# Performance work log

Measured on AMD Instinct MI355X. Metric: run time of the kernel, lower is better.

Reference implementation:

```python
import jax, jax.numpy as jnp
import numpy as np

D_MODEL, D_STATE, D_CONV, EXPAND = 1024, 16, 4, 2
D_INNER = D_MODEL * EXPAND
BATCH, SEQ = 2, 2048


def setup_inputs() -> dict:
    key = jax.random.key(0)
    ks = jax.random.split(key, 10)
    s = lambda d: 1.0 / np.sqrt(d)
    return {
        "x": jax.random.normal(ks[0], (BATCH, SEQ, D_MODEL), jnp.float32),
        "norm_w": jnp.ones((D_MODEL,), jnp.float32),
        "norm_b": jnp.zeros((D_MODEL,), jnp.float32),
        "W_in": jax.random.normal(ks[1], (2 * D_INNER, D_MODEL), jnp.float32) * s(D_MODEL),
        "conv_w": jax.random.normal(ks[2], (D_INNER, D_CONV), jnp.float32) * s(D_CONV),
        "conv_b": jnp.zeros((D_INNER,), jnp.float32),
        "W_dt": jax.random.normal(ks[3], (D_INNER, D_INNER), jnp.float32) * s(D_INNER),
        "b_dt": jnp.zeros((D_INNER,), jnp.float32),
        "W_B": jax.random.normal(ks[4], (D_STATE, D_INNER), jnp.float32) * s(D_INNER),
        "W_C": jax.random.normal(ks[5], (D_STATE, D_INNER), jnp.float32) * s(D_INNER),
        "D": jnp.ones((D_INNER,), jnp.float32),
        "A_log": jnp.broadcast_to(jnp.log(jnp.arange(1, D_STATE + 1, dtype=jnp.float32)), (D_INNER, D_STATE)),
        "W_out": jax.random.normal(ks[6], (D_MODEL, D_INNER), jnp.float32) * s(D_INNER),
    }


def _layernorm(x, w, b, eps=1e-5):
    mu = jnp.mean(x, axis=-1, keepdims=True)
    var = jnp.var(x, axis=-1, keepdims=True)
    return (x - mu) * jax.lax.rsqrt(var + eps) * w + b


def _causal_depthwise_conv(x, w, b):
    # x: [B, L, C], w: [C, K], b: [C]; torch Conv1d(padding=K-1) then slice [:L] == left-pad causal conv
    K = w.shape[1]
    xp = jnp.pad(x, ((0, 0), (K - 1, 0), (0, 0)))
    L = x.shape[1]
    out = b
    for k in range(K):  # small fixed K=4
        out = out + xp[:, k:k + L, :] * w[:, k]
    return out


def reference(x, norm_w, norm_b, W_in, conv_w, conv_b, W_dt, b_dt, W_B, W_C, D, A_log, W_out):
    residual = x
    xn = _layernorm(x, norm_w, norm_b)
    xz = jnp.einsum("bld,ed->ble", xn, W_in)            # [B,L,2*d_inner]
    x_part, z = jnp.split(xz, 2, axis=-1)
    x_conv = jax.nn.silu(_causal_depthwise_conv(x_part, conv_w, conv_b))  # [B,L,di]
    dt = jax.nn.softplus(jnp.einsum("bld,ed->ble", x_conv, W_dt) + b_dt)  # [B,L,di]
    Bm = jnp.einsum("bld,nd->bln", x_conv, W_B)         # [B,L,ds]
    Cm = jnp.einsum("bld,nd->bln", x_conv, W_C)         # [B,L,ds]
    A = -jnp.exp(A_log)                                  # [di,ds]

    def step(h, inp):
        dt_t, B_t, C_t, xc_t = inp                       # [B,di],[B,ds],[B,ds],[B,di]
        h = h * jnp.exp(A[None] * dt_t[:, :, None]) + xc_t[:, :, None] * B_t[:, None, :] * dt_t[:, :, None]
        y_t = jnp.sum(h * C_t[:, None, :], axis=-1)      # [B,di]
        return h, y_t

    h0 = jnp.zeros((x.shape[0], A.shape[0], A.shape[1]), x_conv.dtype)
    # scan over time: move L to leading axis
    xs = (jnp.swapaxes(dt, 0, 1), jnp.swapaxes(Bm, 0, 1), jnp.swapaxes(Cm, 0, 1), jnp.swapaxes(x_conv, 0, 1))
    _, y = jax.lax.scan(step, h0, xs)                    # y: [L,B,di]
    y = jnp.swapaxes(y, 0, 1)
    y = y + x_conv * D
    y = y * jax.nn.silu(z)
    return residual + jnp.einsum("ble,de->bld", y, W_out)
```

## Files before the change

### kernel.cpp

```cpp
#include <hip/hip_runtime.h>
#include <cstdint>
#include <cstddef>

#define D_MODEL 1024
#define D_INNER 2048
#define D_STATE 16
#define SEQ     2048
#define NROWS   4096

typedef short short4v __attribute__((ext_vector_type(4)));
typedef short short8v __attribute__((ext_vector_type(8)));
typedef float float4v __attribute__((ext_vector_type(4)));

__device__ __forceinline__ float bf2f(short u) {
  union { unsigned int i; float f; } v;
  v.i = ((unsigned int)(unsigned short)u) << 16;
  return v.f;
}
__device__ __forceinline__ short f2bf(float f) {
  union { float f; unsigned int i; } v; v.f = f;
  unsigned int r = v.i + 0x7FFFu + ((v.i >> 16) & 1u);
  return (short)(r >> 16);
}
__device__ __forceinline__ float lde(const void* p, size_t i, int f32) {
  return f32 ? ((const float*)p)[i] : bf2f(((const short*)p)[i]);
}
__device__ __forceinline__ void async16(short* lds, const short* g) {
  __builtin_amdgcn_global_load_lds(
      (const __attribute__((address_space(1))) unsigned int*)g,
      (__attribute__((address_space(3))) unsigned int*)lds, 16, 0, 0);
}

__global__ __launch_bounds__(64) void probe_kernel(const unsigned int* __restrict__ xw,
                                                   int* __restrict__ flag) {
  int cnt = 0;
  for (int i = threadIdx.x; i < 1024; i += 64) {
    unsigned e = (xw[i] >> 7) & 0xFFu;
    cnt += (e >= 100u && e <= 150u) ? 1 : 0;
  }
  #pragma unroll
  for (int o = 32; o >= 1; o >>= 1) cnt += __shfl_xor(cnt, o);
  if (threadIdx.x == 0) *flag = (cnt < 614) ? 1 : 0;
}

#define WIN_N  4194304u
#define WDT_N  4194304u
#define WBC_N  32768u
#define WPAD_N 196608u
#define WCAT_N (WDT_N + 2u*WBC_N + WPAD_N)
#define WOUT_N 2097152u
__global__ __launch_bounds__(256) void cvt_kernel(
    const void* __restrict__ Win, const void* __restrict__ Wdt,
    const void* __restrict__ WBp, const void* __restrict__ WCp,
    const void* __restrict__ Wout, short* __restrict__ dst,
    const int* __restrict__ flag) {
  const int f32 = *flag;
  const size_t i = ((size_t)blockIdx.x * 256 + threadIdx.x) * 8;
  const void* src = nullptr; size_t off = 0; bool zero = false;
  if (i < WIN_N) { src = Win; off = i; }
  else {
    size_t j = i - WIN_N;
    if (j < WDT_N) { src = Wdt; off = j; }
    else {
      j -= WDT_N;
      if (j < WBC_N) { src = WBp; off = j; }
      else {
        j -= WBC_N;
        if (j < WBC_N) { src = WCp; off = j; }
        else {
          j -= WBC_N;
          if (j < WPAD_N) zero = true;
          else { src = Wout; off = j - WPAD_N; }
        }
      }
    }
  }
  short8v o;
  if (zero) {
    #pragma unroll
    for (int j = 0; j < 8; ++j) o[j] = 0;
  } else if (f32) {
    const float* s = (const float*)src + off;
    #pragma unroll
    for (int j = 0; j < 8; ++j) o[j] = f2bf(s[j]);
  } else {
    o = *(const short8v*)((const short*)src + off);
  }
  *(short8v*)&dst[i] = o;
}

__global__ __launch_bounds__(256) void ln_kernel(
    const void* __restrict__ x, const void* __restrict__ w,
    const void* __restrict__ bb, short* __restrict__ xn,
    const int* __restrict__ flag) {
  const int f32 = *flag;
  const int row = blockIdx.x;
  const int tid = threadIdx.x;
  float v0, v1, v2, v3;
  if (f32) {
    float4v xv = ((const float4v*)((const float*)x + (size_t)row * D_MODEL))[tid];
    v0 = xv[0]; v1 = xv[1]; v2 = xv[2]; v3 = xv[3];
  } else {
    short4v xv = *(const short4v*)&((const short*)x)[(size_t)row * D_MODEL + tid * 4];
    v0 = bf2f(xv[0]); v1 = bf2f(xv[1]); v2 = bf2f(xv[2]); v3 = bf2f(xv[3]);
  }
  float s = v0 + v1 + v2 + v3;
  float q = v0*v0 + v1*v1 + v2*v2 + v3*v3;
  #pragma unroll
  for (int off = 32; off >= 1; off >>= 1) {
    s += __shfl_xor(s, off);
    q += __shfl_xor(q, off);
  }
  __shared__ float red[8];
  const int wid = tid >> 6;
  if ((tid & 63) == 0) { red[wid] = s; red[4 + wid] = q; }
  __syncthreads();
  s = red[0] + red[1] + red[2] + red[3];
  q = red[4] + red[5] + red[6] + red[7];
  const float mu = s * (1.f / 1024.f);
  const float var = q * (1.f / 1024.f) - mu * mu;
  const float rstd = rsqrtf(var + 1e-5f);
  short4v ov;
  #pragma unroll
  for (int j = 0; j < 4; ++j) {
    const float vj = (j == 0) ? v0 : (j == 1) ? v1 : (j == 2) ? v2 : v3;
    const float o = (vj - mu) * rstd * lde(w, tid * 4 + j, f32) + lde(bb, tid * 4 + j, f32);
    ov[j] = f2bf(o);
  }
  *(short4v*)&xn[(size_t)row * D_MODEL + tid * 4] = ov;
}

template <int MODE, int BM>
__global__ __launch_bounds__(2 * BM) void gemm_bt(
    const short* __restrict__ A, int lda, const short* __restrict__ B,
    void* __restrict__ Cv, int N, int K, const void* __restrict__ aux,
    float* __restrict__ Bmo, float* __restrict__ Cmo,
    const int* __restrict__ flag) {
  constexpr int NBUF = (BM == 256) ? 2 : 4;
  __shared__ __align__(16) short As[NBUF][BM * 32];
  __shared__ __align__(16) short Bs[NBUF][128 * 32];
  const int f32 = *flag;
  const int tid = threadIdx.x;
  const int bm = blockIdx.y * BM;
  const int bn = blockIdx.x << 7;
  const int wid = tid >> 6;
  const int lane = tid & 63;
  const int wm = (wid >> 1) << 6;
  const int wn = (wid & 1) << 6;

  float4v acc[4][4];
  #pragma unroll
  for (int i = 0; i < 4; ++i)
    #pragma unroll
    for (int j = 0; j < 4; ++j) acc[i][j] = (float4v){0.f, 0.f, 0.f, 0.f};

  const int srow = tid >> 2;
  const int scol = (((tid & 3) ^ ((tid >> 3) & 3)) << 3);
  const short* ga = A + (size_t)(bm + srow) * lda + scol;
  const short* gb = B + (size_t)(bn + srow) * K + scol;
  const size_t astep = (size_t)(BM / 2) * lda;
  const size_t bstep = (size_t)64 * K;

  const int fr = lane & 15;
  const int fq = (((lane >> 4) ^ ((lane >> 1) & 3)) << 3);

#define STAGE(Ad, Bd, kk) do {                              \
    async16(&Ad[tid * 8], ga + (kk));                       \
    async16(&Ad[BM * 16 + tid * 8], ga + astep + (kk));     \
    if (BM == 256) {                                        \
      async16(&Bd[tid * 8], gb + (kk));                     \
    } else {                                                \
      async16(&Bd[tid * 8], gb + (kk));                     \
      async16(&Bd[2048 + tid * 8], gb + bstep + (kk));      \
    } } while (0)
#define VMW(NW) __builtin_amdgcn_s_waitcnt(0x3FF0 | (NW))
#define BAR __builtin_amdgcn_s_barrier()

  auto compute = [&](const short* Asrc, const short* Bsrc) {
    short8v af[4], bfv[4];
    #pragma unroll
    for (int i = 0; i < 4; ++i)
      af[i] = *(const short8v*)&Asrc[(wm + i * 16 + fr) * 32 + fq];
    #pragma unroll
    for (int j = 0; j < 4; ++j)
      bfv[j] = *(const short8v*)&Bsrc[(wn + j * 16 + fr) * 32 + fq];
    #pragma unroll
    for (int i = 0; i < 4; ++i)
      #pragma unroll
      for (int j = 0; j < 4; ++j)
        acc[i][j] = __builtin_amdgcn_mfma_f32_16x16x32_bf16(af[i], bfv[j], acc[i][j], 0, 0, 0);
  };

  const int nk = K >> 5;
  if constexpr (BM == 128) {
    STAGE(As[0], Bs[0], 0);
    STAGE(As[1], Bs[1], 32);
    STAGE(As[2], Bs[2], 64);
    int c = 0;
    for (; c + 4 < nk; c += 4) {
      STAGE(As[3], Bs[3], (c + 3) << 5); VMW(12); BAR; compute(As[0], Bs[0]); BAR;
      STAGE(As[0], Bs[0], (c + 4) << 5); VMW(12); BAR; compute(As[1], Bs[1]); BAR;
      STAGE(As[1], Bs[1], (c + 5) << 5); VMW(12); BAR; compute(As[2], Bs[2]); BAR;
      STAGE(As[2], Bs[2], (c + 6) << 5); VMW(12); BAR; compute(As[3], Bs[3]); BAR;
    }
    STAGE(As[3], Bs[3], (nk - 1) << 5); VMW(12); BAR; compute(As[0], Bs[0]); BAR;
    VMW(8); BAR; compute(As[1], Bs[1]); BAR;
    VMW(4); BAR; compute(As[2], Bs[2]); BAR;
    VMW(0); BAR; compute(As[3], Bs[3]);
  } else {
    constexpr int VM3 = 3;
    STAGE(As[0], Bs[0], 0);
    for (int k2 = 0; k2 < nk; k2 += 2) {
      STAGE(As[1], Bs[1], (k2 + 1) << 5);
      VMW(VM3);
      BAR;
      compute(As[0], Bs[0]);
      BAR;
      if (k2 + 2 < nk) {
        STAGE(As[0], Bs[0], (k2 + 2) << 5);
        VMW(VM3);
      } else {
        VMW(0);
      }
      BAR;
      compute(As[1], Bs[1]);
      BAR;
    }
  }
#undef STAGE
#undef VMW
#undef BAR

  const int er = (lane >> 4) << 2;
  const int ec = lane & 15;
  #pragma unroll
  for (int i = 0; i < 4; ++i) {
    #pragma unroll
    for (int j = 0; j < 4; ++j) {
      const int gcol = bn + wn + j * 16 + ec;
      #pragma unroll
      for (int r = 0; r < 4; ++r) {
        const int grow = bm + wm + i * 16 + er + r;
        float v = acc[i][j][r];
        if (MODE == 1) {
          if (gcol < 2048) {
            v += lde(aux, gcol, f32);
            v = (v > 15.f) ? v : log1pf(__expf(v));
            ((short*)Cv)[(size_t)grow * 2048 + gcol] = f2bf(v);
          } else if (gcol < 2064) {
            Bmo[(size_t)grow * 16 + (gcol - 2048)] = v;
          } else if (gcol < 2080) {
            Cmo[(size_t)grow * 16 + (gcol - 2064)] = v;
          }
        } else {
          const size_t idx = (size_t)grow * N + gcol;
          if (MODE == 2) {
            v += lde(aux, idx, f32);
            if (f32) ((float*)Cv)[idx] = v;
            else     ((short*)Cv)[idx] = f2bf(v);
          } else {
            ((short*)Cv)[idx] = f2bf(v);
          }
        }
      }
    }
  }
}

__global__ __launch_bounds__(256) void bc_kernel(
    const short* __restrict__ xcv, const short* __restrict__ wbc,
    float* __restrict__ Bmo, float* __restrict__ Cmo) {
  const int tid = threadIdx.x;
  const int w = tid >> 6;
  const int lane = tid & 63;
  const int fr = lane & 15;
  const int hi = lane >> 4;
  const int r0 = blockIdx.x << 4;
  const short* ap  = xcv + (size_t)(r0 + fr) * 2048 + hi * 8;
  const short* b0p = wbc + (size_t)fr * 2048 + hi * 8;
  const short* b1p = wbc + (size_t)(16 + fr) * 2048 + hi * 8;
  float4v acc0 = (float4v){0.f, 0.f, 0.f, 0.f};
  float4v acc1 = (float4v){0.f, 0.f, 0.f, 0.f};
  #pragma unroll 4
  for (int k = w * 32; k < 2048; k += 128) {
    const short8v af  = *(const short8v*)(ap + k);
    const short8v bf0 = *(const short8v*)(b0p + k);
    const short8v bf1 = *(const short8v*)(b1p + k);
    acc0 = __builtin_amdgcn_mfma_f32_16x16x32_bf16(af, bf0, acc0, 0, 0, 0);
    acc1 = __builtin_amdgcn_mfma_f32_16x16x32_bf16(af, bf1, acc1, 0, 0, 0);
  }
  __shared__ float red[3][64][8];
  if (w) {
    #pragma unroll
    for (int r = 0; r < 4; ++r) {
      red[w - 1][lane][r]     = acc0[r];
      red[w - 1][lane][4 + r] = acc1[r];
    }
  }
  __syncthreads();
  if (w == 0) {
    #pragma unroll
    for (int c = 0; c < 3; ++c)
      #pragma unroll
      for (int r = 0; r < 4; ++r) {
        acc0[r] += red[c][lane][r];
        acc1[r] += red[c][lane][4 + r];
      }
    const int er = hi << 2;
    const int ec = fr;
    #pragma unroll
    for (int r = 0; r < 4; ++r) {
      Bmo[(size_t)(r0 + er + r) * 16 + ec] = acc0[r];
      Cmo[(size_t)(r0 + er + r) * 16 + ec] = acc1[r];
    }
  }
}

#define CONV_RPB 8
__global__ __launch_bounds__(256) void conv_silu(
    const short* __restrict__ xz, const void* __restrict__ cw,
    const void* __restrict__ cb, short* __restrict__ xc,
    const int* __restrict__ flag) {
  const int f32 = *flag;
  const int r0 = blockIdx.x * CONV_RPB;
  const int c0 = threadIdx.x << 3;
  const int t0 = r0 & (SEQ - 1);

  float wreg[32], bias[8];
  if (f32) {
    const float4v* wp = (const float4v*)((const float*)cw + (size_t)c0 * 4);
    #pragma unroll
    for (int q = 0; q < 8; ++q) {
      const float4v v = wp[q];
      #pragma unroll
      for (int k = 0; k < 4; ++k) wreg[q * 4 + k] = v[k];
    }
    const float4v* bp = (const float4v*)((const float*)cb + c0);
    const float4v b0 = bp[0], b1 = bp[1];
    #pragma unroll
    for (int j = 0; j < 4; ++j) { bias[j] = b0[j]; bias[4 + j] = b1[j]; }
  } else {
    const short8v* wp = (const short8v*)((const short*)cw + (size_t)c0 * 4);
    #pragma unroll
    for (int q = 0; q < 4; ++q) {
      const short8v v = wp[q];
      #pragma unroll
      for (int e = 0; e < 8; ++e) wreg[q * 8 + e] = bf2f(v[e]);
    }
    const short8v bv = *(const short8v*)((const short*)cb + c0);
    #pragma unroll
    for (int j = 0; j < 8; ++j) bias[j] = bf2f(bv[j]);
  }

  float xw[4][8];
  #pragma unroll
  for (int k = 0; k < 3; ++k) {
    if (t0 + k - 3 >= 0) {
      const short8v v = *(const short8v*)&xz[(size_t)(r0 + k - 3) * 4096 + c0];
      #pragma unroll
      for (int j = 0; j < 8; ++j) xw[k][j] = bf2f(v[j]);
    } else {
      #pragma unroll
      for (int j = 0; j < 8; ++j) xw[k][j] = 0.f;
    }
  }
  #pragma unroll
  for (int t = 0; t < CONV_RPB; ++t) {
    const int row = r0 + t;
    const short8v v = *(const short8v*)&xz[(size_t)row * 4096 + c0];
    #pragma unroll
    for (int j = 0; j < 8; ++j) xw[3][j] = bf2f(v[j]);
    short8v ov;
    #pragma unroll
    for (int j = 0; j < 8; ++j) {
      float a = bias[j];
      #pragma unroll
      for (int k = 0; k < 4; ++k) a += xw[k][j] * wreg[j * 4 + k];
      ov[j] = f2bf(a / (1.f + __expf(-a)));
    }
    *(short8v*)&xc[(size_t)row * D_INNER + c0] = ov;
    #pragma unroll
    for (int k = 0; k < 3; ++k)
      #pragma unroll
      for (int j = 0; j < 8; ++j) xw[k][j] = xw[k + 1][j];
  }
}

#define SCAN_CK 64
#define SCAN_ST 32
__global__ __launch_bounds__(1024, 4) void scan_kernel(
    const short* __restrict__ dtb, const short* __restrict__ xcv,
    const float* __restrict__ Bm, const float* __restrict__ Cm,
    short* __restrict__ xzb, const void* __restrict__ A_log,
    const void* __restrict__ Dv, const int* __restrict__ flag) {
  const int f32 = *flag;
  const int tid = threadIdx.x;
  const int dl = tid & 15;
  const int ck = tid >> 4;
  const int di = (blockIdx.x << 4) + dl;
  const int b = blockIdx.y;
  const int r0 = (b << 11) + ck * SCAN_ST;

  const short* dtp = dtb + (size_t)r0 * 2048 + di;
  const short* xcp = xcv + (size_t)r0 * 2048 + di;
  const float* bmp = Bm + (size_t)r0 * 16;
  const float* cmp = Cm + (size_t)r0 * 16;
  const short* zp = xzb + (size_t)r0 * 4096 + 2048 + di;
  short* yp = xzb + (size_t)r0 * 4096 + di;

  float Ac[16];
  #pragma unroll
  for (int s = 0; s < 16; ++s)
    Ac[s] = -__expf(lde(A_log, (size_t)di * 16 + s, f32));
  const float Dval = lde(Dv, di, f32);

  bool pat = true;
  #pragma unroll
  for (int s = 1; s < 16; ++s)
    pat = pat && (fabsf(Ac[s] - (float)(s + 1) * Ac[0]) <= fabsf(Ac[s]) * 1e-3f + 1e-6f);
  const float al = Ac[0] * 1.442695041f;

#define POWCHAIN(es, e1) do {                                        \
    es[0] = (e1);                                                    \
    es[1] = es[0] * es[0];  es[2] = es[1] * es[0];                   \
    es[3] = es[1] * es[1];  es[4] = es[3] * es[0];                   \
    es[5] = es[3] * es[1];  es[6] = es[3] * es[2];                   \
    es[7] = es[3] * es[3];  es[8] = es[7] * es[0];                   \
    es[9] = es[7] * es[1];  es[10] = es[7] * es[2];                  \
    es[11] = es[7] * es[3]; es[12] = es[7] * es[4];                  \
    es[13] = es[7] * es[5]; es[14] = es[7] * es[6];                  \
    es[15] = es[7] * es[7]; } while (0)

  float h[16];
  #pragma unroll
  for (int s = 0; s < 16; ++s) h[s] = 0.f;
  float sdt = 0.f;

  if (pat) {
    #pragma unroll 2
    for (int t = 0; t < SCAN_ST; ++t) {
      const float dt = bf2f(dtp[(size_t)t * 2048]);
      const float xc = bf2f(xcp[(size_t)t * 2048]);
      const float4v b0 = *(const float4v*)&bmp[t * 16];
      const float4v b1 = *(const float4v*)&bmp[t * 16 + 4];
      const float4v b2 = *(const float4v*)&bmp[t * 16 + 8];
      const float4v b3 = *(const float4v*)&bmp[t * 16 + 12];
      sdt += dt;
      const float u = xc * dt;
      float es[16];
      POWCHAIN(es, exp2f(al * dt));
      #pragma unroll
      for (int s = 0; s < 4; ++s) {
        h[s]      = h[s]      * es[s]      + u * b0[s];
        h[s + 4]  = h[s + 4]  * es[s + 4]  + u * b1[s];
        h[s + 8]  = h[s + 8]  * es[s + 8]  + u * b2[s];
        h[s + 12] = h[s + 12] * es[s + 12] + u * b3[s];
      }
    }
  } else {
    #pragma unroll 2
    for (int t = 0; t < SCAN_ST; ++t) {
      const float dt = bf2f(dtp[(size_t)t * 2048]);
      const float xc = bf2f(xcp[(size_t)t * 2048]);
      const float4v b0 = *(const float4v*)&bmp[t * 16];
      const float4v b1 = *(const float4v*)&bmp[t * 16 + 4];
      const float4v b2 = *(const float4v*)&bmp[t * 16 + 8];
      const float4v b3 = *(const float4v*)&bmp[t * 16 + 12];
      sdt += dt;
      const float u = xc * dt;
      #pragma unroll
      for (int s = 0; s < 4; ++s) {
        h[s]      = h[s]      * __expf(Ac[s]      * dt) + u * b0[s];
        h[s + 4]  = h[s + 4]  * __expf(Ac[s + 4]  * dt) + u * b1[s];
        h[s + 8]  = h[s + 8]  * __expf(Ac[s + 8]  * dt) + u * b2[s];
        h[s + 12] = h[s + 12] * __expf(Ac[s + 12] * dt) + u * b3[s];
      }
    }
  }

  __shared__ float sdt_s[SCAN_CK][16];
  __shared__ float hc_s[SCAN_CK][16][17];
  sdt_s[ck][dl] = sdt;
  #pragma unroll
  for (int s = 0; s < 16; ++s) hc_s[ck][dl][s] = h[s];
  __syncthreads();
  if (tid < 256) {
    const int s = tid >> 4;
    const float Acs = -__expf(lde(A_log, (size_t)di * 16 + s, f32));
    float hs = 0.f;
    #pragma unroll 4
    for (int c = 0; c < SCAN_CK; ++c) {
      const float hend = hc_s[c][dl][s];
      hc_s[c][dl][s] = hs;
      hs = __expf(Acs * sdt_s[c][dl]) * hs + hend;
    }
  }
  __syncthreads();
  #pragma unroll
  for (int s = 0; s < 16; ++s) h[s] = hc_s[ck][dl][s];

  if (pat) {
    #pragma unroll 2
    for (int t = 0; t < SCAN_ST; ++t) {
      const float dt = bf2f(dtp[(size_t)t * 2048]);
      const float xc = bf2f(xcp[(size_t)t * 2048]);
      const float4v b0 = *(const float4v*)&bmp[t * 16];
      const float4v b1 = *(const float4v*)&bmp[t * 16 + 4];
      const float4v b2 = *(const float4v*)&bmp[t * 16 + 8];
      const float4v b3 = *(const float4v*)&bmp[t * 16 + 12];
      const float4v c0 = *(const float4v*)&cmp[t * 16];
      const float4v c1 = *(const float4v*)&cmp[t * 16 + 4];
      const float4v c2 = *(const float4v*)&cmp[t * 16 + 8];
      const float4v c3 = *(const float4v*)&cmp[t * 16 + 12];
      const float u = xc * dt;
      float es[16];
      POWCHAIN(es, exp2f(al * dt));
      float p0 = 0.f, p1 = 0.f, p2 = 0.f, p3 = 0.f;
      #pragma unroll
      for (int s = 0; s < 4; ++s) {
        h[s]      = h[s]      * es[s]      + u * b0[s];
        h[s + 4]  = h[s + 4]  * es[s + 4]  + u * b1[s];
        h[s + 8]  = h[s + 8]  * es[s + 8]  + u * b2[s];
        h[s + 12] = h[s + 12] * es[s + 12] + u * b3[s];
        p0 += h[s] * c0[s];
        p1 += h[s + 4] * c1[s];
        p2 += h[s + 8] * c2[s];
        p3 += h[s + 12] * c3[s];
      }
      const float p = (p0 + p1) + (p2 + p3);
      const float z = bf2f(zp[(size_t)t * 4096]);
      const float sz = z * __builtin_amdgcn_rcpf(1.f + __expf(-z));
      yp[(size_t)t * 4096] = f2bf((p + xc * Dval) * sz);
    }
  } else {
    #pragma unroll 2
    for (int t = 0; t < SCAN_ST; ++t) {
      const float dt = bf2f(dtp[(size_t)t * 2048]);
      const float xc = bf2f(xcp[(size_t)t * 2048]);
      const float4v b0 = *(const float4v*)&bmp[t * 16];
      const float4v b1 = *(const float4v*)&bmp[t * 16 + 4];
      const float4v b2 = *(const float4v*)&bmp[t * 16 + 8];
      const float4v b3 = *(const float4v*)&bmp[t * 16 + 12];
      const float4v c0 = *(const float4v*)&cmp[t * 16];
      const float4v c1 = *(const float4v*)&cmp[t * 16 + 4];
      const float4v c2 = *(const float4v*)&cmp[t * 16 + 8];
      const float4v c3 = *(const float4v*)&cmp[t * 16 + 12];
      const float u = xc * dt;
      float p0 = 0.f, p1 = 0.f, p2 = 0.f, p3 = 0.f;
      #pragma unroll
      for (int s = 0; s < 4; ++s) {
        h[s]      = h[s]      * __expf(Ac[s]      * dt) + u * b0[s];
        h[s + 4]  = h[s + 4]  * __expf(Ac[s + 4]  * dt) + u * b1[s];
        h[s + 8]  = h[s + 8]  * __expf(Ac[s + 8]  * dt) + u * b2[s];
        h[s + 12] = h[s + 12] * __expf(Ac[s + 12] * dt) + u * b3[s];
        p0 += h[s] * c0[s];
        p1 += h[s + 4] * c1[s];
        p2 += h[s + 8] * c2[s];
        p3 += h[s + 12] * c3[s];
      }
      const float p = (p0 + p1) + (p2 + p3);
      const float z = bf2f(zp[(size_t)t * 4096]);
      const float sz = z * __builtin_amdgcn_rcpf(1.f + __expf(-z));
      yp[(size_t)t * 4096] = f2bf((p + xc * Dval) * sz);
    }
  }
#undef POWCHAIN
}

extern "C" void kernel_launch(void* const* d_in, const int* in_sizes, int n_in,
                              void* d_out, int out_size, void* d_ws, size_t ws_size,
                              hipStream_t stream) {
  const void* x      = d_in[0];
  const void* norm_w = d_in[1];
  const void* norm_b = d_in[2];
  const void* W_in   = d_in[3];
  const void* conv_w = d_in[4];
  const void* conv_b = d_in[5];
  const void* W_dt   = d_in[6];
  const void* b_dt   = d_in[7];
  const void* W_B    = d_in[8];
  const void* W_C    = d_in[9];
  const void* Dv     = d_in[10];
  const void* A_log  = d_in[11];
  const void* W_out  = d_in[12];

  char* ws = (char*)d_ws;
  const size_t MB = (size_t)1 << 20;
  short* wcvt = (short*)(ws);
  short* wbuf = wcvt;
  short* wcat = wcvt + WIN_N;
  short* wout = wcvt + WIN_N + WCAT_N;
  int*   flag = (int*)(ws + 21 * MB - 256);
  short* xzb  = (short*)(ws + 21 * MB);
  short* xcv  = (short*)(ws + 53 * MB);
  short* xn   = (short*)(ws + 69 * MB);
  short* dtb  = (short*)(ws + 69 * MB);
  float* Bm   = (float*)(ws + 85 * MB);
  float* Cm   = Bm + (size_t)NROWS * 16;

  probe_kernel<<<1, 64, 0, stream>>>((const unsigned int*)x, flag);
  cvt_kernel<<<5248, 256, 0, stream>>>(W_in, W_dt, W_B, W_C, W_out, wcvt, flag);
  ln_kernel<<<NROWS, 256, 0, stream>>>(x, norm_w, norm_b, xn, flag);
  gemm_bt<0, 256><<<dim3(32, 16), 512, 0, stream>>>(xn, 1024, wbuf, xzb, 4096, 1024, nullptr, nullptr, nullptr, flag);
  conv_silu<<<NROWS / CONV_RPB, 256, 0, stream>>>(xzb, conv_w, conv_b, xcv, flag);
  gemm_bt<1, 128><<<dim3(16, 32), 256, 0, stream>>>(xcv, 2048, wcat, dtb, 2176, 2048, b_dt, nullptr, nullptr, flag);
  bc_kernel<<<256, 256, 0, stream>>>(xcv, wcat + (size_t)2048 * 2048, Bm, Cm);
  scan_kernel<<<dim3(128, 2), 1024, 0, stream>>>(dtb, xcv, Bm, Cm, xzb, A_log, Dv, flag);
  gemm_bt<2, 128><<<dim3(8, 32), 256, 0, stream>>>(xzb, 4096, wout, d_out, 1024, 2048, x, nullptr, nullptr, flag);
}
```

Measured before the change: 379.8 us.

## Fold B/C projection into dt GEMM and remap scan blocks across XCDs

Removes the separate bc_kernel and widens the dt GEMM grid from 16 to 17 column tiles so the extra tile writes B and C projections through the existing epilogue path. The scan launch becomes a 1D grid with a block index swizzle that spreads consecutive channel groups across chiplets. This saves a kernel launch and a second read of the conv output, at the cost of one partially used GEMM tile column.

```diff
diff --git a/kernel.cpp b/kernel.cpp
--- a/kernel.cpp
+++ b/kernel.cpp
@@ -208,17 +208,16 @@
     VMW(4); BAR; compute(As[2], Bs[2]); BAR;
     VMW(0); BAR; compute(As[3], Bs[3]);
   } else {
-    constexpr int VM3 = 3;
     STAGE(As[0], Bs[0], 0);
     for (int k2 = 0; k2 < nk; k2 += 2) {
       STAGE(As[1], Bs[1], (k2 + 1) << 5);
-      VMW(VM3);
+      VMW(3);
       BAR;
       compute(As[0], Bs[0]);
       BAR;
       if (k2 + 2 < nk) {
         STAGE(As[0], Bs[0], (k2 + 2) << 5);
-        VMW(VM3);
+        VMW(3);
       } else {
         VMW(0);
       }
@@ -267,55 +266,6 @@
   }
 }
 
-__global__ __launch_bounds__(256) void bc_kernel(
-    const short* __restrict__ xcv, const short* __restrict__ wbc,
-    float* __restrict__ Bmo, float* __restrict__ Cmo) {
-  const int tid = threadIdx.x;
-  const int w = tid >> 6;
-  const int lane = tid & 63;
-  const int fr = lane & 15;
-  const int hi = lane >> 4;
-  const int r0 = blockIdx.x << 4;
-  const short* ap  = xcv + (size_t)(r0 + fr) * 2048 + hi * 8;
-  const short* b0p = wbc + (size_t)fr * 2048 + hi * 8;
-  const short* b1p = wbc + (size_t)(16 + fr) * 2048 + hi * 8;
-  float4v acc0 = (float4v){0.f, 0.f, 0.f, 0.f};
-  float4v acc1 = (float4v){0.f, 0.f, 0.f, 0.f};
-  #pragma unroll 4
-  for (int k = w * 32; k < 2048; k += 128) {
-    const short8v af  = *(const short8v*)(ap + k);
-    const short8v bf0 = *(const short8v*)(b0p + k);
-    const short8v bf1 = *(const short8v*)(b1p + k);
-    acc0 = __builtin_amdgcn_mfma_f32_16x16x32_bf16(af, bf0, acc0, 0, 0, 0);
-    acc1 = __builtin_amdgcn_mfma_f32_16x16x32_bf16(af, bf1, acc1, 0, 0, 0);
-  }
-  __shared__ float red[3][64][8];
-  if (w) {
-    #pragma unroll
-    for (int r = 0; r < 4; ++r) {
-      red[w - 1][lane][r]     = acc0[r];
-      red[w - 1][lane][4 + r] = acc1[r];
-    }
-  }
-  __syncthreads();
-  if (w == 0) {
-    #pragma unroll
-    for (int c = 0; c < 3; ++c)
-      #pragma unroll
-      for (int r = 0; r < 4; ++r) {
-        acc0[r] += red[c][lane][r];
-        acc1[r] += red[c][lane][4 + r];
-      }
-    const int er = hi << 2;
-    const int ec = fr;
-    #pragma unroll
-    for (int r = 0; r < 4; ++r) {
-      Bmo[(size_t)(r0 + er + r) * 16 + ec] = acc0[r];
-      Cmo[(size_t)(r0 + er + r) * 16 + ec] = acc1[r];
-    }
-  }
-}
-
 #define CONV_RPB 8
 __global__ __launch_bounds__(256) void conv_silu(
     const short* __restrict__ xz, const void* __restrict__ cw,
@@ -397,8 +347,11 @@
   const int tid = threadIdx.x;
   const int dl = tid & 15;
   const int ck = tid >> 4;
-  const int di = (blockIdx.x << 4) + dl;
-  const int b = blockIdx.y;
+  const int d = blockIdx.x;
+  const int s_ = ((d & 7) << 5) | (d >> 3);
+  const int bx = s_ & 127;
+  const int b = s_ >> 7;
+  const int di = (bx << 4) + dl;
   const int r0 = (b << 11) + ck * SCAN_ST;
 
   const short* dtp = dtb + (size_t)r0 * 2048 + di;
@@ -603,8 +556,7 @@
   ln_kernel<<<NROWS, 256, 0, stream>>>(x, norm_w, norm_b, xn, flag);
   gemm_bt<0, 256><<<dim3(32, 16), 512, 0, stream>>>(xn, 1024, wbuf, xzb, 4096, 1024, nullptr, nullptr, nullptr, flag);
   conv_silu<<<NROWS / CONV_RPB, 256, 0, stream>>>(xzb, conv_w, conv_b, xcv, flag);
-  gemm_bt<1, 128><<<dim3(16, 32), 256, 0, stream>>>(xcv, 2048, wcat, dtb, 2176, 2048, b_dt, nullptr, nullptr, flag);
-  bc_kernel<<<256, 256, 0, stream>>>(xcv, wcat + (size_t)2048 * 2048, Bm, Cm);
-  scan_kernel<<<dim3(128, 2), 1024, 0, stream>>>(dtb, xcv, Bm, Cm, xzb, A_log, Dv, flag);
+  gemm_bt<1, 128><<<dim3(17, 32), 256, 0, stream>>>(xcv, 2048, wcat, dtb, 2176, 2048, b_dt, Bm, Cm, flag);
+  scan_kernel<<<256, 1024, 0, stream>>>(dtb, xcv, Bm, Cm, xzb, A_log, Dv, flag);
   gemm_bt<2, 128><<<dim3(8, 32), 256, 0, stream>>>(xzb, 4096, wout, d_out, 1024, 2048, x, nullptr, nullptr, flag);
 }
```

Result: slower. 412.4 us (+8.6%).
